# Kernel tuning notes

Hardware: AMD Instinct MI355X
Metric: run time of the kernel (lower is better)

The kernel has to match this reference:

```python
import jax, jax.numpy as jnp
import numpy as np

N_NODES = 10000
N_EDGES = 640000
EMB_DIM = 128
NUM_LAYERS = 4
EPS_GIN = 0.0   # Tokenizer init eps
BN_EPS = 1e-5


def setup_inputs() -> dict:
    key = jax.random.key(0)
    k1, k2, k3 = jax.random.split(key, 3)
    x = jax.random.normal(k1, (N_NODES, EMB_DIM), dtype=jnp.float32)
    src = jax.random.randint(k2, (N_EDGES,), 0, N_NODES)
    dst = jax.random.randint(k3, (N_EDGES,), 0, N_NODES)
    gamma = jnp.ones((NUM_LAYERS, EMB_DIM), dtype=jnp.float32)
    beta = jnp.zeros((NUM_LAYERS, EMB_DIM), dtype=jnp.float32)
    return {"x": x, "gamma": gamma, "beta": beta, "src": src, "dst": dst}


def reference(x, gamma, beta, src, dst):
    # Tokenizer forward: num_layer x (NonParaGINConv -> BatchNorm1d), JK='last'
    n = x.shape[0]
    h = x
    for l in range(NUM_LAYERS):
        # GIN: neigh = sum over in-edges of source features (copy_u + fn.sum)
        neigh = jax.ops.segment_sum(h[src], dst, num_segments=n)
        h = (1.0 + EPS_GIN) * h + neigh
        # BatchNorm1d, training mode: biased batch statistics over nodes
        mu = jnp.mean(h, axis=0)
        var = jnp.var(h, axis=0)
        h = (h - mu) * jax.lax.rsqrt(var + BN_EPS) * gamma[l] + beta[l]
    return h  # JK == 'last'
```

## Files before the change

kernel.cpp:

```cpp
#include <hip/hip_runtime.h>

#define DIM 128
#define BN_EPS_F 1e-5f
#define NSLICE 16
#define MAXN 10240
#define CHUNKS 128

typedef unsigned int u32;
typedef unsigned short u16;

__device__ __forceinline__ float bflo(u32 w) {
    union { u32 u; float f; } c; c.u = w << 16; return c.f;
}
__device__ __forceinline__ float bfhi(u32 w) {
    union { u32 u; float f; } c; c.u = w & 0xffff0000u; return c.f;
}
__device__ __forceinline__ u32 packbf(float x, float y) {
    union { float f; u32 u; } ax, ay; ax.f = x; ay.f = y;
    u32 xr = (ax.u + 0x7fffu + ((ax.u >> 16) & 1u)) >> 16;
    u32 yr = (ay.u + 0x7fffu + ((ay.u >> 16) & 1u)) >> 16;
    return xr | (yr << 16);
}

__device__ __forceinline__ void addrow(float* acc, const uint4 v) {
    acc[0] += bflo(v.x); acc[1] += bfhi(v.x);
    acc[2] += bflo(v.y); acc[3] += bfhi(v.y);
    acc[4] += bflo(v.z); acc[5] += bfhi(v.z);
    acc[6] += bflo(v.w); acc[7] += bfhi(v.w);
}


__global__ __launch_bounds__(256) void chunkhist_kernel(const int* __restrict__ dst,
                                                        int* __restrict__ hist,
                                                        int n, int E, int chunk) {
    __shared__ int bins[MAXN];
    int tid = threadIdx.x;
    for (int i = tid; i < n; i += 256) bins[i] = 0;
    __syncthreads();
    int e0 = blockIdx.x * chunk;
    int e1 = min(e0 + chunk, E);
    for (int e = e0 + tid; e < e1; e += 256) atomicAdd(&bins[dst[e]], 1);
    __syncthreads();
    int* out = hist + (size_t)blockIdx.x * n;
    for (int i = tid; i < n; i += 256) out[i] = bins[i];
}

__global__ __launch_bounds__(256) void chunkscan_kernel(const int* __restrict__ hist,
                                                        int* __restrict__ chunkpref,
                                                        int* __restrict__ counts, int n) {
    int bin = blockIdx.x * 256 + threadIdx.x;
    if (bin >= n) return;
    const int* hp = hist + bin;
    int* cp = chunkpref + bin;
    int run = 0;
#pragma unroll 32
    for (int b = 0; b < CHUNKS; b++) {
        int v = hp[(size_t)b * n];
        cp[(size_t)b * n] = run;
        run += v;
    }
    counts[bin] = run;
}

__global__ __launch_bounds__(1024) void scan_kernel(const int* __restrict__ counts,
                                                    int* __restrict__ prowptr, int n) {
    __shared__ int sums[1024];
    const int CH = 16;
    int t = threadIdx.x;
    int base = t * CH;
    int local[CH];
    int s = 0;
#pragma unroll
    for (int i = 0; i < CH; i++) {
        int idx = base + i;
        local[i] = s;
        if (idx < n) s += (counts[idx] + 15) & ~15;
    }
    sums[t] = s;
    __syncthreads();
    for (int off = 1; off < 1024; off <<= 1) {
        int v = (t >= off) ? sums[t - off] : 0;
        __syncthreads();
        sums[t] += v;
        __syncthreads();
    }
    int prev = (t > 0) ? sums[t - 1] : 0;
#pragma unroll
    for (int i = 0; i < CH; i++) {
        int idx = base + i;
        if (idx < n) prowptr[idx] = prev + local[i];
    }
    if (t == 1023) prowptr[n] = sums[1023];
}

__global__ __launch_bounds__(256) void misc_kernel(const float* __restrict__ x,
                                                   u16* __restrict__ xb,
                                                   u16* __restrict__ r0,
                                                   u16* __restrict__ r1,
                                                   const int* __restrict__ prowptr,
                                                   const int* __restrict__ counts,
                                                   int* __restrict__ srcsorted,
                                                   float* __restrict__ gstats,
                                                   int total4, int n,
                                                   int nb_cvt, int nb_pad, int gtotal) {
    int bid = blockIdx.x;
    int tid = threadIdx.x;
    if (bid < nb_cvt) {
        int i = bid * 256 + tid;
        if (i < total4) {
            float4 v = ((const float4*)x)[i];
            uint2 w;
            w.x = packbf(v.x, v.y);
            w.y = packbf(v.z, v.w);
            *(uint2*)(xb + (size_t)i * 4) = w;
        } else {
            int j = i - total4;
            if (j < 96) {
                u16* t = (j < 32) ? xb : ((j < 64) ? r0 : r1);
                uint2 z; z.x = 0; z.y = 0;
                *(uint2*)(t + (size_t)n * DIM + (j & 31) * 4) = z;
            }
        }
    } else if (bid < nb_cvt + nb_pad) {
        int i = (bid - nb_cvt) * 256 + tid;
        if (i < n) {
            int pstart = prowptr[i];
            int c = counts[i];
            int p = (c + 15) & ~15;
            for (int k = c; k < p; k++) srcsorted[pstart + k] = n;
        }
    } else {
        int i = (bid - nb_cvt - nb_pad) * 256 + tid;
        if (i < gtotal) gstats[i] = 0.f;
    }
}

__global__ __launch_bounds__(256) void scatter_kernel(const int* __restrict__ src,
                                                      const int* __restrict__ dst,
                                                      const int* __restrict__ prowptr,
                                                      const int* __restrict__ chunkpref,
                                                      int* __restrict__ srcsorted,
                                                      int n, int E, int chunk) {
    __shared__ int cur[MAXN];
    int tid = threadIdx.x;
    const int* cp = chunkpref + (size_t)blockIdx.x * n;
    for (int i = tid; i < n; i += 256) cur[i] = prowptr[i] + cp[i];
    __syncthreads();
    int e0 = blockIdx.x * chunk;
    int e1 = min(e0 + chunk, E);
    for (int e = e0 + tid; e < e1; e += 256) {
        int d = dst[e];
        int pos = atomicAdd(&cur[d], 1);
        srcsorted[pos] = src[e];
    }
}

template <int USE_AB>
__global__ __launch_bounds__(256, 4) void gather_kernel(
    const u16* __restrict__ hin, u16* __restrict__ hout,
    const int* __restrict__ prowptr, const int* __restrict__ counts,
    const int* __restrict__ srcs,
    const float* __restrict__ stats_in, float* __restrict__ stats_out,
    const float* __restrict__ gamma, const float* __restrict__ beta,
    int n, int ngroups, float inv_n) {
    __shared__ float ab_s[2 * DIM];
    __shared__ float part[2][DIM];
    __shared__ float ls[4][DIM];
    __shared__ float lq[4][DIM];
    int tid = threadIdx.x;
    int wid = tid >> 6;
    int lane = tid & 63;
    int grp = lane >> 4;
    int sub = lane & 15;

    if (USE_AB) {
        int c = tid & 127;
        int which = tid >> 7;
        const float* basep = stats_in + which * NSLICE * DIM + c;
        float acc = 0.f;
#pragma unroll
        for (int k = 0; k < NSLICE; k++) acc += basep[k * DIM];
        part[which][c] = acc;
        __syncthreads();
        if (tid < DIM) {
            float mu = part[0][tid] * inv_n;
            float var = part[1][tid] * inv_n - mu * mu;
            float av = gamma[tid] * rsqrtf(var + BN_EPS_F);
            ab_s[tid] = av;
            ab_s[DIM + tid] = beta[tid] - mu * av;
        }
        __syncthreads();
    }

    float sacc[8], qacc[8];
#pragma unroll
    for (int k = 0; k < 8; k++) { sacc[k] = 0.f; qacc[k] = 0.f; }

    for (int g = blockIdx.x; g < ngroups; g += gridDim.x) {
        int node = g * 4 + wid;
        if (node >= n) continue;
        int start = prowptr[node];
        int pend = prowptr[node + 1];
        int deg = counts[node];
        const u16* hsub = hin + sub * 8;
        float acc[8];
#pragma unroll
        for (int k = 0; k < 8; k++) acc[k] = 0.f;

        int eb = start;
        if (eb + 32 <= pend) {
            int e0 = eb + grp * 4;
            int s0 = srcs[e0 + 0], s1 = srcs[e0 + 1];
            int s2 = srcs[e0 + 2], s3 = srcs[e0 + 3];
            int s4 = srcs[e0 + 16], s5 = srcs[e0 + 17];
            int s6 = srcs[e0 + 18], s7 = srcs[e0 + 19];
            while (true) {
                uint4 v0 = *(const uint4*)(hsub + (size_t)s0 * DIM);
                uint4 v1 = *(const uint4*)(hsub + (size_t)s1 * DIM);
                uint4 v2 = *(const uint4*)(hsub + (size_t)s2 * DIM);
                uint4 v3 = *(const uint4*)(hsub + (size_t)s3 * DIM);
                uint4 v4 = *(const uint4*)(hsub + (size_t)s4 * DIM);
                uint4 v5 = *(const uint4*)(hsub + (size_t)s5 * DIM);
                uint4 v6 = *(const uint4*)(hsub + (size_t)s6 * DIM);
                uint4 v7 = *(const uint4*)(hsub + (size_t)s7 * DIM);
                int nb = eb + 32;
                if (nb + 32 <= pend) {
                    int e1 = nb + grp * 4;
                    s0 = srcs[e1 + 0]; s1 = srcs[e1 + 1];
                    s2 = srcs[e1 + 2]; s3 = srcs[e1 + 3];
                    s4 = srcs[e1 + 16]; s5 = srcs[e1 + 17];
                    s6 = srcs[e1 + 18]; s7 = srcs[e1 + 19];
                }
                addrow(acc, v0); addrow(acc, v1);
                addrow(acc, v2); addrow(acc, v3);
                addrow(acc, v4); addrow(acc, v5);
                addrow(acc, v6); addrow(acc, v7);
                eb = nb;
                if (eb + 32 > pend) break;
            }
        }
        if (eb < pend) {
            int e0 = eb + grp * 4;
            int s0 = srcs[e0 + 0], s1 = srcs[e0 + 1];
            int s2 = srcs[e0 + 2], s3 = srcs[e0 + 3];
            uint4 v0 = *(const uint4*)(hsub + (size_t)s0 * DIM);
            uint4 v1 = *(const uint4*)(hsub + (size_t)s1 * DIM);
            uint4 v2 = *(const uint4*)(hsub + (size_t)s2 * DIM);
            uint4 v3 = *(const uint4*)(hsub + (size_t)s3 * DIM);
            addrow(acc, v0); addrow(acc, v1);
            addrow(acc, v2); addrow(acc, v3);
        }
#pragma unroll
        for (int k = 0; k < 8; k++) {
            acc[k] += __shfl_xor(acc[k], 16);
            acc[k] += __shfl_xor(acc[k], 32);
        }

        uint4 sv = *(const uint4*)(hin + (size_t)node * DIM + sub * 8);
        float self[8] = {bflo(sv.x), bfhi(sv.x), bflo(sv.y), bfhi(sv.y),
                         bflo(sv.z), bfhi(sv.z), bflo(sv.w), bfhi(sv.w)};
        float degp1 = 1.0f + (float)deg;

        float o[8];
        if (USE_AB) {
            float4 a0 = *(const float4*)(ab_s + sub * 8);
            float4 a1 = *(const float4*)(ab_s + sub * 8 + 4);
            float4 b0 = *(const float4*)(ab_s + DIM + sub * 8);
            float4 b1 = *(const float4*)(ab_s + DIM + sub * 8 + 4);
            o[0] = a0.x * (self[0] + acc[0]) + degp1 * b0.x;
            o[1] = a0.y * (self[1] + acc[1]) + degp1 * b0.y;
            o[2] = a0.z * (self[2] + acc[2]) + degp1 * b0.z;
            o[3] = a0.w * (self[3] + acc[3]) + degp1 * b0.w;
            o[4] = a1.x * (self[4] + acc[4]) + degp1 * b1.x;
            o[5] = a1.y * (self[5] + acc[5]) + degp1 * b1.y;
            o[6] = a1.z * (self[6] + acc[6]) + degp1 * b1.z;
            o[7] = a1.w * (self[7] + acc[7]) + degp1 * b1.w;
        } else {
#pragma unroll
            for (int k = 0; k < 8; k++) o[k] = self[k] + acc[k];
        }
        u32 w0 = packbf(o[0], o[1]);
        u32 w1 = packbf(o[2], o[3]);
        u32 w2 = packbf(o[4], o[5]);
        u32 w3 = packbf(o[6], o[7]);
        if (grp == 0) {
            uint4 wv; wv.x = w0; wv.y = w1; wv.z = w2; wv.w = w3;
            *(uint4*)(hout + (size_t)node * DIM + sub * 8) = wv;
        }
        float rr[8] = {bflo(w0), bfhi(w0), bflo(w1), bfhi(w1),
                       bflo(w2), bfhi(w2), bflo(w3), bfhi(w3)};
#pragma unroll
        for (int k = 0; k < 8; k++) {
            sacc[k] += rr[k];
            qacc[k] += rr[k] * rr[k];
        }
    }

    __syncthreads();
    if (grp == 0) {
#pragma unroll
        for (int k = 0; k < 8; k++) {
            ls[wid][sub * 8 + k] = sacc[k];
            lq[wid][sub * 8 + k] = qacc[k];
        }
    }
    __syncthreads();
    int slice = (blockIdx.x & (NSLICE - 1)) * DIM;
    int c = tid & 127;
    int which = tid >> 7;
    float s = which ? ((lq[0][c] + lq[1][c]) + (lq[2][c] + lq[3][c]))
                    : ((ls[0][c] + ls[1][c]) + (ls[2][c] + ls[3][c]));
    atomicAdd(&stats_out[which * NSLICE * DIM + slice + c], s);
}

__global__ __launch_bounds__(256) void apply_kernel(const u16* __restrict__ hb,
                                                    const float* __restrict__ stats_in,
                                                    const float* __restrict__ gamma,
                                                    const float* __restrict__ beta,
                                                    float* __restrict__ out, int total4,
                                                    float inv_n) {
    __shared__ float ab_s[2 * DIM];
    __shared__ float part[2][DIM];
    int tid = threadIdx.x;
    {
        int c = tid & 127;
        int which = tid >> 7;
        const float* basep = stats_in + which * NSLICE * DIM + c;
        float acc = 0.f;
#pragma unroll
        for (int k = 0; k < NSLICE; k++) acc += basep[k * DIM];
        part[which][c] = acc;
        __syncthreads();
        if (tid < DIM) {
            float mu = part[0][tid] * inv_n;
            float var = part[1][tid] * inv_n - mu * mu;
            float av = gamma[tid] * rsqrtf(var + BN_EPS_F);
            ab_s[tid] = av;
            ab_s[DIM + tid] = beta[tid] - mu * av;
        }
        __syncthreads();
    }
    for (int i = blockIdx.x * blockDim.x + tid; i < total4; i += gridDim.x * blockDim.x) {
        int quad = i & 31;
        uint2 w = *(const uint2*)(hb + (size_t)i * 4);
        const float4 a = *(const float4*)(ab_s + quad * 4);
        const float4 b = *(const float4*)(ab_s + DIM + quad * 4);
        float4 r;
        r.x = a.x * bflo(w.x) + b.x;
        r.y = a.y * bfhi(w.x) + b.y;
        r.z = a.z * bflo(w.y) + b.z;
        r.w = a.w * bfhi(w.y) + b.w;
        ((float4*)out)[i] = r;
    }
}

extern "C" void kernel_launch(void* const* d_in, const int* in_sizes, int n_in,
                              void* d_out, int out_size, void* d_ws, size_t ws_size,
                              hipStream_t stream) {
    const float* x = (const float*)d_in[0];
    const float* gamma = (const float*)d_in[1];
    const float* beta = (const float*)d_in[2];
    const int* src = (const int*)d_in[3];
    const int* dst = (const int*)d_in[4];
    float* out = (float*)d_out;

    const int n = in_sizes[0] / DIM;
    const int E = in_sizes[3];

    char* ws = (char*)d_ws;
    auto alloc = [&](size_t bytes) -> char* {
        char* p = ws;
        ws += (bytes + 255) / 256 * 256;
        return p;
    };
    const int STATS_PER_LAYER = 2 * NSLICE * DIM;
    int* prowptr = (int*)alloc((size_t)(n + 1) * 4);
    int* counts = (int*)alloc((size_t)n * 4);
    float* gstats = (float*)alloc((size_t)4 * STATS_PER_LAYER * 4);
    int* hist = (int*)alloc((size_t)CHUNKS * n * 4);
    int* chunkpref = (int*)alloc((size_t)CHUNKS * n * 4);
    int* srcsorted = (int*)alloc((size_t)(E + 16 * n) * 4);
    u16* hbx = (u16*)alloc((size_t)(n + 1) * DIM * 2);
    u16* hb0 = (u16*)alloc((size_t)(n + 1) * DIM * 2);
    u16* hb1 = (u16*)alloc((size_t)(n + 1) * DIM * 2);

    const int chunk = (E + CHUNKS - 1) / CHUNKS;
    const int total4 = n * DIM / 4;
    const int gtotal = 4 * STATS_PER_LAYER;
    const int NB_CVT = (total4 + 96 + 255) / 256;
    const int NB_PAD = (n + 255) / 256;
    const int NB_GZ = (gtotal + 255) / 256;

    chunkhist_kernel<<<CHUNKS, 256, 0, stream>>>(dst, hist, n, E, chunk);
    chunkscan_kernel<<<(n + 255) / 256, 256, 0, stream>>>(hist, chunkpref, counts, n);
    scan_kernel<<<1, 1024, 0, stream>>>(counts, prowptr, n);
    misc_kernel<<<NB_CVT + NB_PAD + NB_GZ, 256, 0, stream>>>(x, hbx, hb0, hb1, prowptr,
                                                             counts, srcsorted, gstats,
                                                             total4, n, NB_CVT, NB_PAD,
                                                             gtotal);
    scatter_kernel<<<CHUNKS, 256, 0, stream>>>(src, dst, prowptr, chunkpref, srcsorted,
                                               n, E, chunk);

    const int ngroups = (n + 3) / 4;
    const int GB = (ngroups + 1) / 2;
    const float inv_n = 1.0f / n;
    float* st0 = gstats + 0 * STATS_PER_LAYER;
    float* st1 = gstats + 1 * STATS_PER_LAYER;
    float* st2 = gstats + 2 * STATS_PER_LAYER;
    float* st3 = gstats + 3 * STATS_PER_LAYER;

    gather_kernel<0><<<GB, 256, 0, stream>>>(hbx, hb0, prowptr, counts, srcsorted,
                                             nullptr, st0, nullptr, nullptr, n, ngroups,
                                             inv_n);
    gather_kernel<1><<<GB, 256, 0, stream>>>(hb0, hb1, prowptr, counts, srcsorted,
                                             st0, st1, gamma + 0 * DIM, beta + 0 * DIM,
                                             n, ngroups, inv_n);
    gather_kernel<1><<<GB, 256, 0, stream>>>(hb1, hb0, prowptr, counts, srcsorted,
                                             st1, st2, gamma + 1 * DIM, beta + 1 * DIM,
                                             n, ngroups, inv_n);
    gather_kernel<1><<<GB, 256, 0, stream>>>(hb0, hb1, prowptr, counts, srcsorted,
                                             st2, st3, gamma + 2 * DIM, beta + 2 * DIM,
                                             n, ngroups, inv_n);
    apply_kernel<<<256, 256, 0, stream>>>(hb1, st3, gamma + 3 * DIM, beta + 3 * DIM, out,
                                          total4, inv_n);
}
```

Baseline: 185.7 us.

## Fuse conversion, GIN layers and final BN into one cooperative persistent kernel

```diff
diff --git a/kernel.cpp b/kernel.cpp
--- a/kernel.cpp
+++ b/kernel.cpp
@@ -1,10 +1,14 @@
 #include <hip/hip_runtime.h>
+#include <hip/hip_cooperative_groups.h>
+
+namespace cg = cooperative_groups;
 
 #define DIM 128
 #define BN_EPS_F 1e-5f
 #define NSLICE 16
 #define MAXN 10240
-#define CHUNKS 128
+#define CHUNKS 256
+#define SPL (2 * NSLICE * DIM)
 
 typedef unsigned int u32;
 typedef unsigned short u16;
@@ -91,48 +95,6 @@
         if (idx < n) prowptr[idx] = prev + local[i];
     }
     if (t == 1023) prowptr[n] = sums[1023];
-}
-
-__global__ __launch_bounds__(256) void misc_kernel(const float* __restrict__ x,
-                                                   u16* __restrict__ xb,
-                                                   u16* __restrict__ r0,
-                                                   u16* __restrict__ r1,
-                                                   const int* __restrict__ prowptr,
-                                                   const int* __restrict__ counts,
-                                                   int* __restrict__ srcsorted,
-                                                   float* __restrict__ gstats,
-                                                   int total4, int n,
-                                                   int nb_cvt, int nb_pad, int gtotal) {
-    int bid = blockIdx.x;
-    int tid = threadIdx.x;
-    if (bid < nb_cvt) {
-        int i = bid * 256 + tid;
-        if (i < total4) {
-            float4 v = ((const float4*)x)[i];
-            uint2 w;
-            w.x = packbf(v.x, v.y);
-            w.y = packbf(v.z, v.w);
-            *(uint2*)(xb + (size_t)i * 4) = w;
-        } else {
-            int j = i - total4;
-            if (j < 96) {
-                u16* t = (j < 32) ? xb : ((j < 64) ? r0 : r1);
-                uint2 z; z.x = 0; z.y = 0;
-                *(uint2*)(t + (size_t)n * DIM + (j & 31) * 4) = z;
-            }
-        }
-    } else if (bid < nb_cvt + nb_pad) {
-        int i = (bid - nb_cvt) * 256 + tid;
-        if (i < n) {
-            int pstart = prowptr[i];
-            int c = counts[i];
-            int p = (c + 15) & ~15;
-            for (int k = c; k < p; k++) srcsorted[pstart + k] = n;
-        }
-    } else {
-        int i = (bid - nb_cvt - nb_pad) * 256 + tid;
-        if (i < gtotal) gstats[i] = 0.f;
-    }
 }
 
 __global__ __launch_bounds__(256) void scatter_kernel(const int* __restrict__ src,
@@ -155,66 +117,94 @@
     }
 }
 
-template <int USE_AB>
-__global__ __launch_bounds__(256, 4) void gather_kernel(
-    const u16* __restrict__ hin, u16* __restrict__ hout,
+__global__ __launch_bounds__(256, 4) void mega_kernel(
+    const float* __restrict__ x, u16* __restrict__ hbx,
+    u16* __restrict__ hb0, u16* __restrict__ hb1,
     const int* __restrict__ prowptr, const int* __restrict__ counts,
-    const int* __restrict__ srcs,
-    const float* __restrict__ stats_in, float* __restrict__ stats_out,
+    int* __restrict__ srcs, float* __restrict__ gstats,
     const float* __restrict__ gamma, const float* __restrict__ beta,
-    int n, int ngroups, float inv_n) {
+    float* __restrict__ out, int n, int total4, float inv_n) {
+    cg::grid_group grid = cg::this_grid();
     __shared__ float ab_s[2 * DIM];
     __shared__ float part[2][DIM];
     __shared__ float ls[4][DIM];
     __shared__ float lq[4][DIM];
     int tid = threadIdx.x;
+    int gsize = gridDim.x * 256;
+    int gidx0 = blockIdx.x * 256 + tid;
     int wid = tid >> 6;
     int lane = tid & 63;
     int grp = lane >> 4;
     int sub = lane & 15;
 
-    if (USE_AB) {
-        int c = tid & 127;
-        int which = tid >> 7;
-        const float* basep = stats_in + which * NSLICE * DIM + c;
-        float acc = 0.f;
-#pragma unroll
-        for (int k = 0; k < NSLICE; k++) acc += basep[k * DIM];
-        part[which][c] = acc;
-        __syncthreads();
-        if (tid < DIM) {
-            float mu = part[0][tid] * inv_n;
-            float var = part[1][tid] * inv_n - mu * mu;
-            float av = gamma[tid] * rsqrtf(var + BN_EPS_F);
-            ab_s[tid] = av;
-            ab_s[DIM + tid] = beta[tid] - mu * av;
-        }
-        __syncthreads();
-    }
-
-    float sacc[8], qacc[8];
-#pragma unroll
-    for (int k = 0; k < 8; k++) { sacc[k] = 0.f; qacc[k] = 0.f; }
-
-    for (int g = blockIdx.x; g < ngroups; g += gridDim.x) {
-        int node = g * 4 + wid;
-        if (node >= n) continue;
-        int start = prowptr[node];
-        int pend = prowptr[node + 1];
-        int deg = counts[node];
-        const u16* hsub = hin + sub * 8;
-        float acc[8];
-#pragma unroll
-        for (int k = 0; k < 8; k++) acc[k] = 0.f;
-
-        int eb = start;
-        if (eb + 32 <= pend) {
-            int e0 = eb + grp * 4;
-            int s0 = srcs[e0 + 0], s1 = srcs[e0 + 1];
-            int s2 = srcs[e0 + 2], s3 = srcs[e0 + 3];
-            int s4 = srcs[e0 + 16], s5 = srcs[e0 + 17];
-            int s6 = srcs[e0 + 18], s7 = srcs[e0 + 19];
-            while (true) {
+    for (int i = gidx0; i < total4; i += gsize) {
+        float4 v = ((const float4*)x)[i];
+        uint2 w;
+        w.x = packbf(v.x, v.y);
+        w.y = packbf(v.z, v.w);
+        *(uint2*)(hbx + (size_t)i * 4) = w;
+    }
+    if (gidx0 < 96) {
+        u16* t = (gidx0 < 32) ? hbx : ((gidx0 < 64) ? hb0 : hb1);
+        uint2 z; z.x = 0; z.y = 0;
+        *(uint2*)(t + (size_t)n * DIM + (gidx0 & 31) * 4) = z;
+    }
+    for (int i = gidx0; i < n; i += gsize) {
+        int pstart = prowptr[i];
+        int c = counts[i];
+        int p = (c + 15) & ~15;
+        for (int k = c; k < p; k++) srcs[pstart + k] = n;
+    }
+    for (int i = gidx0; i < 4 * SPL; i += gsize) gstats[i] = 0.f;
+    grid.sync();
+
+    const u16* hin = hbx;
+    u16* houts[4] = {hb0, hb1, hb0, hb1};
+    for (int l = 0; l < 4; l++) {
+        u16* hout = houts[l];
+        float* st_out = gstats + l * SPL;
+        if (l > 0) {
+            const float* st_in = gstats + (l - 1) * SPL;
+            int c = tid & 127;
+            int which = tid >> 7;
+            const float* basep = st_in + which * NSLICE * DIM + c;
+            float acc = 0.f;
+#pragma unroll
+            for (int k = 0; k < NSLICE; k++) acc += basep[k * DIM];
+            part[which][c] = acc;
+            __syncthreads();
+            if (tid < DIM) {
+                float mu = part[0][tid] * inv_n;
+                float var = part[1][tid] * inv_n - mu * mu;
+                float av = gamma[(l - 1) * DIM + tid] * rsqrtf(var + BN_EPS_F);
+                ab_s[tid] = av;
+                ab_s[DIM + tid] = beta[(l - 1) * DIM + tid] - mu * av;
+            }
+            __syncthreads();
+        }
+
+        float sacc[8], qacc[8];
+#pragma unroll
+        for (int k = 0; k < 8; k++) { sacc[k] = 0.f; qacc[k] = 0.f; }
+
+        for (int node0 = blockIdx.x * 4; node0 < n; node0 += gridDim.x * 4) {
+            int node = node0 + wid;
+            if (node >= n) continue;
+            int start = prowptr[node];
+            int pend = prowptr[node + 1];
+            int deg = counts[node];
+            const u16* hsub = hin + sub * 8;
+            float acc[8];
+#pragma unroll
+            for (int k = 0; k < 8; k++) acc[k] = 0.f;
+
+            int eb = start;
+            for (; eb + 32 <= pend; eb += 32) {
+                int e0 = eb + grp * 4;
+                int s0 = srcs[e0 + 0], s1 = srcs[e0 + 1];
+                int s2 = srcs[e0 + 2], s3 = srcs[e0 + 3];
+                int s4 = srcs[e0 + 16], s5 = srcs[e0 + 17];
+                int s6 = srcs[e0 + 18], s7 = srcs[e0 + 19];
                 uint4 v0 = *(const uint4*)(hsub + (size_t)s0 * DIM);
                 uint4 v1 = *(const uint4*)(hsub + (size_t)s1 * DIM);
                 uint4 v2 = *(const uint4*)(hsub + (size_t)s2 * DIM);
@@ -223,109 +213,92 @@
                 uint4 v5 = *(const uint4*)(hsub + (size_t)s5 * DIM);
                 uint4 v6 = *(const uint4*)(hsub + (size_t)s6 * DIM);
                 uint4 v7 = *(const uint4*)(hsub + (size_t)s7 * DIM);
-                int nb = eb + 32;
-                if (nb + 32 <= pend) {
-                    int e1 = nb + grp * 4;
-                    s0 = srcs[e1 + 0]; s1 = srcs[e1 + 1];
-                    s2 = srcs[e1 + 2]; s3 = srcs[e1 + 3];
-                    s4 = srcs[e1 + 16]; s5 = srcs[e1 + 17];
-                    s6 = srcs[e1 + 18]; s7 = srcs[e1 + 19];
-                }
                 addrow(acc, v0); addrow(acc, v1);
                 addrow(acc, v2); addrow(acc, v3);
                 addrow(acc, v4); addrow(acc, v5);
                 addrow(acc, v6); addrow(acc, v7);
-                eb = nb;
-                if (eb + 32 > pend) break;
-            }
-        }
-        if (eb < pend) {
-            int e0 = eb + grp * 4;
-            int s0 = srcs[e0 + 0], s1 = srcs[e0 + 1];
-            int s2 = srcs[e0 + 2], s3 = srcs[e0 + 3];
-            uint4 v0 = *(const uint4*)(hsub + (size_t)s0 * DIM);
-            uint4 v1 = *(const uint4*)(hsub + (size_t)s1 * DIM);
-            uint4 v2 = *(const uint4*)(hsub + (size_t)s2 * DIM);
-            uint4 v3 = *(const uint4*)(hsub + (size_t)s3 * DIM);
-            addrow(acc, v0); addrow(acc, v1);
-            addrow(acc, v2); addrow(acc, v3);
-        }
-#pragma unroll
-        for (int k = 0; k < 8; k++) {
-            acc[k] += __shfl_xor(acc[k], 16);
-            acc[k] += __shfl_xor(acc[k], 32);
-        }
-
-        uint4 sv = *(const uint4*)(hin + (size_t)node * DIM + sub * 8);
-        float self[8] = {bflo(sv.x), bfhi(sv.x), bflo(sv.y), bfhi(sv.y),
-                         bflo(sv.z), bfhi(sv.z), bflo(sv.w), bfhi(sv.w)};
-        float degp1 = 1.0f + (float)deg;
-
-        float o[8];
-        if (USE_AB) {
-            float4 a0 = *(const float4*)(ab_s + sub * 8);
-            float4 a1 = *(const float4*)(ab_s + sub * 8 + 4);
-            float4 b0 = *(const float4*)(ab_s + DIM + sub * 8);
-            float4 b1 = *(const float4*)(ab_s + DIM + sub * 8 + 4);
-            o[0] = a0.x * (self[0] + acc[0]) + degp1 * b0.x;
-            o[1] = a0.y * (self[1] + acc[1]) + degp1 * b0.y;
-            o[2] = a0.z * (self[2] + acc[2]) + degp1 * b0.z;
-            o[3] = a0.w * (self[3] + acc[3]) + degp1 * b0.w;
-            o[4] = a1.x * (self[4] + acc[4]) + degp1 * b1.x;
-            o[5] = a1.y * (self[5] + acc[5]) + degp1 * b1.y;
-            o[6] = a1.z * (self[6] + acc[6]) + degp1 * b1.z;
-            o[7] = a1.w * (self[7] + acc[7]) + degp1 * b1.w;
-        } else {
-#pragma unroll
-            for (int k = 0; k < 8; k++) o[k] = self[k] + acc[k];
-        }
-        u32 w0 = packbf(o[0], o[1]);
-        u32 w1 = packbf(o[2], o[3]);
-        u32 w2 = packbf(o[4], o[5]);
-        u32 w3 = packbf(o[6], o[7]);
+            }
+            if (eb < pend) {
+                int e0 = eb + grp * 4;
+                int s0 = srcs[e0 + 0], s1 = srcs[e0 + 1];
+                int s2 = srcs[e0 + 2], s3 = srcs[e0 + 3];
+                uint4 v0 = *(const uint4*)(hsub + (size_t)s0 * DIM);
+                uint4 v1 = *(const uint4*)(hsub + (size_t)s1 * DIM);
+                uint4 v2 = *(const uint4*)(hsub + (size_t)s2 * DIM);
+                uint4 v3 = *(const uint4*)(hsub + (size_t)s3 * DIM);
+                addrow(acc, v0); addrow(acc, v1);
+                addrow(acc, v2); addrow(acc, v3);
+            }
+#pragma unroll
+            for (int k = 0; k < 8; k++) {
+                acc[k] += __shfl_xor(acc[k], 16);
+                acc[k] += __shfl_xor(acc[k], 32);
+            }
+
+            uint4 sv = *(const uint4*)(hin + (size_t)node * DIM + sub * 8);
+            float self[8] = {bflo(sv.x), bfhi(sv.x), bflo(sv.y), bfhi(sv.y),
+                             bflo(sv.z), bfhi(sv.z), bflo(sv.w), bfhi(sv.w)};
+            float degp1 = 1.0f + (float)deg;
+
+            float o[8];
+            if (l > 0) {
+                float4 a0 = *(const float4*)(ab_s + sub * 8);
+                float4 a1 = *(const float4*)(ab_s + sub * 8 + 4);
+                float4 b0 = *(const float4*)(ab_s + DIM + sub * 8);
+                float4 b1 = *(const float4*)(ab_s + DIM + sub * 8 + 4);
+                o[0] = a0.x * (self[0] + acc[0]) + degp1 * b0.x;
+                o[1] = a0.y * (self[1] + acc[1]) + degp1 * b0.y;
+                o[2] = a0.z * (self[2] + acc[2]) + degp1 * b0.z;
+                o[3] = a0.w * (self[3] + acc[3]) + degp1 * b0.w;
+                o[4] = a1.x * (self[4] + acc[4]) + degp1 * b1.x;
+                o[5] = a1.y * (self[5] + acc[5]) + degp1 * b1.y;
+                o[6] = a1.z * (self[6] + acc[6]) + degp1 * b1.z;
+                o[7] = a1.w * (self[7] + acc[7]) + degp1 * b1.w;
+            } else {
+#pragma unroll
+                for (int k = 0; k < 8; k++) o[k] = self[k] + acc[k];
+            }
+            u32 w0 = packbf(o[0], o[1]);
+            u32 w1 = packbf(o[2], o[3]);
+            u32 w2 = packbf(o[4], o[5]);
+            u32 w3 = packbf(o[6], o[7]);
+            if (grp == 0) {
+                uint4 wv; wv.x = w0; wv.y = w1; wv.z = w2; wv.w = w3;
+                *(uint4*)(hout + (size_t)node * DIM + sub * 8) = wv;
+            }
+            float rr[8] = {bflo(w0), bfhi(w0), bflo(w1), bfhi(w1),
+                           bflo(w2), bfhi(w2), bflo(w3), bfhi(w3)};
+#pragma unroll
+            for (int k = 0; k < 8; k++) {
+                sacc[k] += rr[k];
+                qacc[k] += rr[k] * rr[k];
+            }
+        }
+
+        __syncthreads();
         if (grp == 0) {
-            uint4 wv; wv.x = w0; wv.y = w1; wv.z = w2; wv.w = w3;
-            *(uint4*)(hout + (size_t)node * DIM + sub * 8) = wv;
-        }
-        float rr[8] = {bflo(w0), bfhi(w0), bflo(w1), bfhi(w1),
-                       bflo(w2), bfhi(w2), bflo(w3), bfhi(w3)};
-#pragma unroll
-        for (int k = 0; k < 8; k++) {
-            sacc[k] += rr[k];
-            qacc[k] += rr[k] * rr[k];
-        }
-    }
-
-    __syncthreads();
-    if (grp == 0) {
-#pragma unroll
-        for (int k = 0; k < 8; k++) {
-            ls[wid][sub * 8 + k] = sacc[k];
-            lq[wid][sub * 8 + k] = qacc[k];
-        }
-    }
-    __syncthreads();
-    int slice = (blockIdx.x & (NSLICE - 1)) * DIM;
-    int c = tid & 127;
-    int which = tid >> 7;
-    float s = which ? ((lq[0][c] + lq[1][c]) + (lq[2][c] + lq[3][c]))
-                    : ((ls[0][c] + ls[1][c]) + (ls[2][c] + ls[3][c]));
-    atomicAdd(&stats_out[which * NSLICE * DIM + slice + c], s);
-}
-
-__global__ __launch_bounds__(256) void apply_kernel(const u16* __restrict__ hb,
-                                                    const float* __restrict__ stats_in,
-                                                    const float* __restrict__ gamma,
-                                                    const float* __restrict__ beta,
-                                                    float* __restrict__ out, int total4,
-                                                    float inv_n) {
-    __shared__ float ab_s[2 * DIM];
-    __shared__ float part[2][DIM];
-    int tid = threadIdx.x;
+#pragma unroll
+            for (int k = 0; k < 8; k++) {
+                ls[wid][sub * 8 + k] = sacc[k];
+                lq[wid][sub * 8 + k] = qacc[k];
+            }
+        }
+        __syncthreads();
+        int slice = (blockIdx.x & (NSLICE - 1)) * DIM;
+        int c2 = tid & 127;
+        int which2 = tid >> 7;
+        float sflush = which2 ? ((lq[0][c2] + lq[1][c2]) + (lq[2][c2] + lq[3][c2]))
+                              : ((ls[0][c2] + ls[1][c2]) + (ls[2][c2] + ls[3][c2]));
+        atomicAdd(&st_out[which2 * NSLICE * DIM + slice + c2], sflush);
+        grid.sync();
+        hin = hout;
+    }
+
     {
+        const float* st_in = gstats + 3 * SPL;
         int c = tid & 127;
         int which = tid >> 7;
-        const float* basep = stats_in + which * NSLICE * DIM + c;
+        const float* basep = st_in + which * NSLICE * DIM + c;
         float acc = 0.f;
 #pragma unroll
         for (int k = 0; k < NSLICE; k++) acc += basep[k * DIM];
@@ -334,23 +307,24 @@
         if (tid < DIM) {
             float mu = part[0][tid] * inv_n;
             float var = part[1][tid] * inv_n - mu * mu;
-            float av = gamma[tid] * rsqrtf(var + BN_EPS_F);
+            float av = gamma[3 * DIM + tid] * rsqrtf(var + BN_EPS_F);
             ab_s[tid] = av;
-            ab_s[DIM + tid] = beta[tid] - mu * av;
-        }
-        __syncthreads();
-    }
-    for (int i = blockIdx.x * blockDim.x + tid; i < total4; i += gridDim.x * blockDim.x) {
-        int quad = i & 31;
-        uint2 w = *(const uint2*)(hb + (size_t)i * 4);
-        const float4 a = *(const float4*)(ab_s + quad * 4);
-        const float4 b = *(const float4*)(ab_s + DIM + quad * 4);
-        float4 r;
-        r.x = a.x * bflo(w.x) + b.x;
-        r.y = a.y * bfhi(w.x) + b.y;
-        r.z = a.z * bflo(w.y) + b.z;
-        r.w = a.w * bfhi(w.y) + b.w;
-        ((float4*)out)[i] = r;
+            ab_s[DIM + tid] = beta[3 * DIM + tid] - mu * av;
+        }
+        __syncthreads();
+        const u16* hb = hin;
+        for (int i = gidx0; i < total4; i += gsize) {
+            int quad = i & 31;
+            uint2 w = *(const uint2*)(hb + (size_t)i * 4);
+            const float4 a = *(const float4*)(ab_s + quad * 4);
+            const float4 b = *(const float4*)(ab_s + DIM + quad * 4);
+            float4 r;
+            r.x = a.x * bflo(w.x) + b.x;
+            r.y = a.y * bfhi(w.x) + b.y;
+            r.z = a.z * bflo(w.y) + b.z;
+            r.w = a.w * bfhi(w.y) + b.w;
+            ((float4*)out)[i] = r;
+        }
     }
 }
 
@@ -373,10 +347,9 @@
         ws += (bytes + 255) / 256 * 256;
         return p;
     };
-    const int STATS_PER_LAYER = 2 * NSLICE * DIM;
     int* prowptr = (int*)alloc((size_t)(n + 1) * 4);
     int* counts = (int*)alloc((size_t)n * 4);
-    float* gstats = (float*)alloc((size_t)4 * STATS_PER_LAYER * 4);
+    float* gstats = (float*)alloc((size_t)4 * SPL * 4);
     int* hist = (int*)alloc((size_t)CHUNKS * n * 4);
     int* chunkpref = (int*)alloc((size_t)CHUNKS * n * 4);
     int* srcsorted = (int*)alloc((size_t)(E + 16 * n) * 4);
@@ -386,41 +359,28 @@
 
     const int chunk = (E + CHUNKS - 1) / CHUNKS;
     const int total4 = n * DIM / 4;
-    const int gtotal = 4 * STATS_PER_LAYER;
-    const int NB_CVT = (total4 + 96 + 255) / 256;
-    const int NB_PAD = (n + 255) / 256;
-    const int NB_GZ = (gtotal + 255) / 256;
+    const float inv_n = 1.0f / n;
 
     chunkhist_kernel<<<CHUNKS, 256, 0, stream>>>(dst, hist, n, E, chunk);
     chunkscan_kernel<<<(n + 255) / 256, 256, 0, stream>>>(hist, chunkpref, counts, n);
     scan_kernel<<<1, 1024, 0, stream>>>(counts, prowptr, n);
-    misc_kernel<<<NB_CVT + NB_PAD + NB_GZ, 256, 0, stream>>>(x, hbx, hb0, hb1, prowptr,
-                                                             counts, srcsorted, gstats,
-                                                             total4, n, NB_CVT, NB_PAD,
-                                                             gtotal);
     scatter_kernel<<<CHUNKS, 256, 0, stream>>>(src, dst, prowptr, chunkpref, srcsorted,
                                                n, E, chunk);
 
-    const int ngroups = (n + 3) / 4;
-    const int GB = (ngroups + 1) / 2;
-    const float inv_n = 1.0f / n;
-    float* st0 = gstats + 0 * STATS_PER_LAYER;
-    float* st1 = gstats + 1 * STATS_PER_LAYER;
-    float* st2 = gstats + 2 * STATS_PER_LAYER;
-    float* st3 = gstats + 3 * STATS_PER_LAYER;
-
-    gather_kernel<0><<<GB, 256, 0, stream>>>(hbx, hb0, prowptr, counts, srcsorted,
-                                             nullptr, st0, nullptr, nullptr, n, ngroups,
-                                             inv_n);
-    gather_kernel<1><<<GB, 256, 0, stream>>>(hb0, hb1, prowptr, counts, srcsorted,
-                                             st0, st1, gamma + 0 * DIM, beta + 0 * DIM,
-                                             n, ngroups, inv_n);
-    gather_kernel<1><<<GB, 256, 0, stream>>>(hb1, hb0, prowptr, counts, srcsorted,
-                                             st1, st2, gamma + 1 * DIM, beta + 1 * DIM,
-                                             n, ngroups, inv_n);
-    gather_kernel<1><<<GB, 256, 0, stream>>>(hb0, hb1, prowptr, counts, srcsorted,
-                                             st2, st3, gamma + 2 * DIM, beta + 2 * DIM,
-                                             n, ngroups, inv_n);
-    apply_kernel<<<256, 256, 0, stream>>>(hb1, st3, gamma + 3 * DIM, beta + 3 * DIM, out,
-                                          total4, inv_n);
-}
+    hipDeviceProp_t prop;
+    hipGetDeviceProperties(&prop, 0);
+    int nbPerCU = 0;
+    hipOccupancyMaxActiveBlocksPerMultiprocessor(&nbPerCU, mega_kernel, 256, 0);
+    if (nbPerCU < 1) nbPerCU = 1;
+    long long gb = (long long)nbPerCU * prop.multiProcessorCount;
+    if (gb > 2048) gb = 2048;
+    int GB = (int)gb;
+
+    int n_ = n, total4_ = total4;
+    float inv_n_ = inv_n;
+    void* kargs[] = {(void*)&x, (void*)&hbx, (void*)&hb0, (void*)&hb1,
+                     (void*)&prowptr, (void*)&counts, (void*)&srcsorted,
+                     (void*)&gstats, (void*)&gamma, (void*)&beta,
+                     (void*)&out, (void*)&n_, (void*)&total4_, (void*)&inv_n_};
+    hipLaunchCooperativeKernel((void*)mega_kernel, dim3(GB), dim3(256), kargs, 0, stream);
+}
```

New measurement: 496.3 us. 167% more time.
